# Performance work log

Measured on AMD Instinct MI355X. Metric: run time of the kernel, lower is better.

The kernel has to match this reference:

```python
import jax, jax.numpy as jnp
import numpy as np

# Module constants (from init_kwargs / source constants)
BEV_H, BEV_W = 188, 126
IMG_H, IMG_W = 384, 768
X_MIN, X_MAX = 0.0, 75.2
Y_MIN, Y_MAX = -25.2, 25.2


def _bev_points():
    """Homogeneous car-frame BEV cell centers, [P,4] with P = BEV_H*BEV_W, Z=0."""
    dx = (X_MAX - X_MIN) / BEV_H
    dy = (Y_MAX - Y_MIN) / BEV_W
    xc = jnp.linspace(X_MIN + dx / 2.0, X_MAX - dx / 2.0, BEV_H)
    yc = jnp.linspace(Y_MIN + dy / 2.0, Y_MAX - dy / 2.0, BEV_W)
    X, Y = jnp.meshgrid(xc, yc, indexing='ij')
    P = BEV_H * BEV_W
    return jnp.stack([X.ravel(), Y.ravel(), jnp.zeros(P), jnp.ones(P)], axis=-1)


def setup_inputs() -> dict:
    key = jax.random.key(0)
    k1, k2, k3 = jax.random.split(key, 3)
    B, N, C, Hf, Wf = 2, 6, 256, 48, 96
    feats = jax.random.normal(k1, (B, N, C, Hf, Wf), dtype=jnp.float32)
    # Realistic intrinsics: fx=fy=500, principal point at image center, + small noise
    K_base = jnp.array([[500.0, 0.0, IMG_W / 2.0],
                        [0.0, 500.0, IMG_H / 2.0],
                        [0.0, 0.0, 1.0]], dtype=jnp.float32)
    intrinsics = K_base[None, None] + 5.0 * jax.random.normal(k2, (B, N, 3, 3), dtype=jnp.float32)
    intrinsics = intrinsics.at[..., 2, :].set(jnp.array([0.0, 0.0, 1.0]))
    # Extrinsics: car x (forward) -> cam z, car y -> -cam x, car z (up) -> -cam y,
    # camera 1.5m above ground; small per-camera perturbation so cams differ.
    M_base = jnp.array([[0.0, -1.0, 0.0, 0.0],
                        [0.0, 0.0, -1.0, 1.5],
                        [1.0, 0.0, 0.0, 0.0],
                        [0.0, 0.0, 0.0, 1.0]], dtype=jnp.float32)
    car_to_cam = M_base[None, None] + 0.01 * jax.random.normal(k3, (B, N, 4, 4), dtype=jnp.float32)
    car_to_cam = car_to_cam.at[..., 3, :].set(jnp.array([0.0, 0.0, 0.0, 1.0]))
    return {"feats": feats, "intrinsics": intrinsics, "car_to_cam": car_to_cam}


def _forward(feats, intrinsics, car_to_cam):
    B, N, C, Hf, Wf = feats.shape
    P_car = _bev_points().astype(feats.dtype)  # [P,4]
    # Per-camera projection of BEV points into camera frame: P_cam = P_car @ M^T
    P_cam = jnp.einsum('pk,bnjk->bnpj', P_car, car_to_cam)  # [B,N,P,4]
    Zc = P_cam[..., 2]
    valid = Zc > 0.1
    # Pinhole projection: p_img = K @ P_cam3
    p_img = jnp.einsum('bnij,bnpj->bnpi', intrinsics, P_cam[..., :3])  # [B,N,P,3]
    z = jnp.maximum(p_img[..., 2], 1e-4)
    u_feat = (p_img[..., 0] / z) / (IMG_W / float(Wf))
    v_feat = (p_img[..., 1] / z) / (IMG_H / float(Hf))
    valid = valid & (u_feat >= 0.0) & (u_feat <= Wf - 1.0) & (v_feat >= 0.0) & (v_feat <= Hf - 1.0)
    u_norm = jnp.where(valid, u_feat / (Wf - 1) * 2.0 - 1.0, 2.0)
    v_norm = jnp.where(valid, v_feat / (Hf - 1) * 2.0 - 1.0, 2.0)
    # grid_sample, bilinear, padding_mode='zeros', align_corners=True
    ix = (u_norm + 1.0) * 0.5 * (Wf - 1)  # [B,N,P]
    iy = (v_norm + 1.0) * 0.5 * (Hf - 1)
    x0 = jnp.floor(ix)
    y0 = jnp.floor(iy)
    wx1 = ix - x0
    wx0 = 1.0 - wx1
    wy1 = iy - y0
    wy0 = 1.0 - wy1
    feats_flat = feats.reshape(B, N, C, Hf * Wf)

    def gather(xf, yf):
        inb = (xf >= 0) & (xf <= Wf - 1) & (yf >= 0) & (yf <= Hf - 1)
        xi = jnp.clip(xf, 0, Wf - 1).astype(jnp.int32)
        yi = jnp.clip(yf, 0, Hf - 1).astype(jnp.int32)
        lin = yi * Wf + xi  # [B,N,P]
        val = jnp.take_along_axis(feats_flat, lin[:, :, None, :], axis=3)  # [B,N,C,P]
        return val * inb[:, :, None, :].astype(val.dtype)

    out = (gather(x0, y0) * (wx0 * wy0)[:, :, None, :]
           + gather(x0 + 1.0, y0) * (wx1 * wy0)[:, :, None, :]
           + gather(x0, y0 + 1.0) * (wx0 * wy1)[:, :, None, :]
           + gather(x0 + 1.0, y0 + 1.0) * (wx1 * wy1)[:, :, None, :])  # [B,N,C,P]
    bev = out.mean(axis=1).reshape(B, C, BEV_H, BEV_W)
    return bev


def reference(feats, intrinsics, car_to_cam):
    return _forward(feats, intrinsics, car_to_cam)
```

## Files before the change

### kernel.cpp

```cpp
#include <hip/hip_runtime.h>

namespace {

constexpr int kBevH = 188, kBevW = 126, kP = kBevH * kBevW;
constexpr int kB = 2, kN = 6, kC = 256, kHf = 48, kWf = 96;
constexpr int kHW = kHf * kWf;
constexpr int kPixBytes = kC * 2;
constexpr int kPTile = 32;
constexpr int kNTiles = (kP + kPTile - 1) / kPTile;
constexpr size_t kImgBytes = (size_t)kB * kN * kHW * kC * 2;
constexpr size_t kWsNeeded = kImgBytes;

typedef float vfloat4 __attribute__((ext_vector_type(4)));

__device__ __forceinline__ unsigned short f2bf(float f) {
  union { float f; unsigned u; } a; a.f = f;
  unsigned r = a.u + 0x7fffu + ((a.u >> 16) & 1u);
  return (unsigned short)(r >> 16);
}
__device__ __forceinline__ float bfl(unsigned u) {
  union { unsigned u; float f; } a; a.u = u << 16; return a.f;
}
__device__ __forceinline__ float bfh(unsigned u) {
  union { unsigned u; float f; } a; a.u = u & 0xffff0000u; return a.f;
}

__global__ __launch_bounds__(256) void transpose_cvt_kernel(
    const float* __restrict__ src, unsigned short* __restrict__ dst) {
  __shared__ float tile[64][33];
  const int m = blockIdx.z;
  const int hw0 = blockIdx.x * 32;
  const int c0 = blockIdx.y * 64;
  const float* s = src + (size_t)m * kC * kHW;
  unsigned short* d = dst + (size_t)m * kHW * kC;
  const int hw = threadIdx.x & 31, cl = threadIdx.x >> 5;
#pragma unroll
  for (int k = 0; k < 8; ++k)
    tile[cl + 8 * k][hw] = s[(size_t)(c0 + cl + 8 * k) * kHW + hw0 + hw];
  __syncthreads();
  const int cp = threadIdx.x & 31, hwl = threadIdx.x >> 5;
#pragma unroll
  for (int k = 0; k < 4; ++k) {
    const int h = hwl + 8 * k;
    ushort2 uv;
    uv.x = f2bf(tile[2 * cp][h]);
    uv.y = f2bf(tile[2 * cp + 1][h]);
    *(ushort2*)(d + (size_t)(hw0 + h) * kC + c0 + 2 * cp) = uv;
  }
}

__global__ __launch_bounds__(512) void gather_kernel(
    const unsigned char* __restrict__ tf, const float* __restrict__ intr,
    const float* __restrict__ c2c, float* __restrict__ out) {
  __shared__ float sm[kPTile][261];
  __shared__ int2 s_off[kPTile][kN];
  __shared__ float4 s_wt[kPTile][kN];

  const int b = blockIdx.y;
  const int orig = blockIdx.x;
  constexpr int q = kNTiles / 8, r = kNTiles % 8;
  const int xcd = orig & 7, idx = orig >> 3;
  const int tile = (xcd < r ? xcd * (q + 1) : r * (q + 1) + (xcd - r) * q) + idx;
  const int p0 = tile * kPTile;
  const int tid = threadIdx.x;

  if (tid < kPTile * kN) {
    const int pl = tid / kN, n = tid - pl * kN;
    const int p = min(p0 + pl, kP - 1);
    const int pi = p / kBevW, pj = p - pi * kBevW;
    const float dxc = 75.2f / 188.0f, dyc = 50.4f / 126.0f;
    const float xcar = 0.5f * dxc + (float)pi * dxc;
    const float ycar = -25.2f + 0.5f * dyc + (float)pj * dyc;
    const float* M = c2c + ((size_t)b * kN + n) * 16;
    const float* K = intr + ((size_t)b * kN + n) * 9;
    float Xc = M[0] * xcar + M[1] * ycar + M[3];
    float Yc = M[4] * xcar + M[5] * ycar + M[7];
    float Zc = M[8] * xcar + M[9] * ycar + M[11];
    float u = K[0] * Xc + K[1] * Yc + K[2] * Zc;
    float v = K[3] * Xc + K[4] * Yc + K[5] * Zc;
    float w = K[6] * Xc + K[7] * Yc + K[8] * Zc;
    float z = fmaxf(w, 1e-4f);
    float uf = (u / z) * 0.125f;
    float vf = (v / z) * 0.125f;
    bool valid = (Zc > 0.1f) && (uf >= 0.0f) && (uf <= 95.0f) &&
                 (vf >= 0.0f) && (vf <= 47.0f);
    int2 ov = make_int2(0, 0);
    float4 wv = make_float4(0.f, 0.f, 0.f, 0.f);
    if (valid) {
      float un = (uf / 95.0f) * 2.0f - 1.0f;
      float vn = (vf / 47.0f) * 2.0f - 1.0f;
      float ix = (un + 1.0f) * 0.5f * 95.0f;
      float iy = (vn + 1.0f) * 0.5f * 47.0f;
      float x0f = floorf(ix), y0f = floorf(iy);
      float wx1 = ix - x0f, wx0 = 1.0f - wx1;
      float wy1 = iy - y0f, wy0 = 1.0f - wy1;
      int x0i = (int)x0f;
      int y0i = (int)y0f;
      int xb = min(x0i, 94);
      float h0 = (x0i <= 94) ? wx0 : 0.0f;
      float h1 = (x0i <= 94) ? wx1 : wx0;
      int y1i = min(y0i + 1, 47);
      const int pix = (b * kN + n) * kHW;
      ov.x = (pix + y0i * kWf + xb) * kPixBytes;
      ov.y = (pix + y1i * kWf + xb) * kPixBytes;
      wv = make_float4(h0 * wy0, h1 * wy0, h0 * wy1, h1 * wy1);
    }
    s_off[pl][n] = ov;
    s_wt[pl][n] = wv;
  }
  __syncthreads();

  const int w = tid >> 6, l = tid & 63;
  const int half = l >> 5;
  const int l16 = l << 4;
  const float inv_n = 1.0f / 6.0f;

#pragma unroll
  for (int j = 0; j < 4; ++j) {
    const int pl = w * 4 + j;

    const int2 o0 = s_off[pl][0], o1 = s_off[pl][1], o2 = s_off[pl][2],
               o3 = s_off[pl][3], o4 = s_off[pl][4], o5 = s_off[pl][5];
    const float4 q0 = s_wt[pl][0], q1 = s_wt[pl][1], q2 = s_wt[pl][2],
                 q3 = s_wt[pl][3], q4 = s_wt[pl][4], q5 = s_wt[pl][5];

#define LD(nm, o) \
    const uint4 nm##a = *(const uint4*)(tf + (size_t)o.x + l16); \
    const uint4 nm##b = *(const uint4*)(tf + (size_t)o.y + l16);
    LD(d0, o0) LD(d1, o1) LD(d2, o2) LD(d3, o3) LD(d4, o4) LD(d5, o5)
#undef LD

    float a0 = 0.f, a1 = 0.f, a2 = 0.f, a3 = 0.f,
          a4 = 0.f, a5 = 0.f, a6 = 0.f, a7 = 0.f;
#define CAM(da, db, wv) { \
    const float selA = half ? wv.y : wv.x; \
    const float selB = half ? wv.w : wv.z; \
    a0 += selA * bfl(da.x) + selB * bfl(db.x); \
    a1 += selA * bfh(da.x) + selB * bfh(db.x); \
    a2 += selA * bfl(da.y) + selB * bfl(db.y); \
    a3 += selA * bfh(da.y) + selB * bfh(db.y); \
    a4 += selA * bfl(da.z) + selB * bfl(db.z); \
    a5 += selA * bfh(da.z) + selB * bfh(db.z); \
    a6 += selA * bfl(da.w) + selB * bfl(db.w); \
    a7 += selA * bfh(da.w) + selB * bfh(db.w); }
    CAM(d0a, d0b, q0) CAM(d1a, d1b, q1) CAM(d2a, d2b, q2)
    CAM(d3a, d3b, q3) CAM(d4a, d4b, q4) CAM(d5a, d5b, q5)
#undef CAM

    a0 += __shfl_xor(a0, 32); a1 += __shfl_xor(a1, 32);
    a2 += __shfl_xor(a2, 32); a3 += __shfl_xor(a3, 32);
    a4 += __shfl_xor(a4, 32); a5 += __shfl_xor(a5, 32);
    a6 += __shfl_xor(a6, 32); a7 += __shfl_xor(a7, 32);

    const int cbase = ((l & 31) << 3) + (half << 2);
    float4 vs = half ? make_float4(a4, a5, a6, a7)
                     : make_float4(a0, a1, a2, a3);
    vs.x *= inv_n; vs.y *= inv_n; vs.z *= inv_n; vs.w *= inv_n;
    *(float4*)&sm[pl][cbase] = vs;
  }
  __syncthreads();

#pragma unroll
  for (int rd = 0; rd < 4; ++rd) {
    const int cr = rd * 64 + (tid >> 3);
    const int p4 = (tid & 7) * 4;
    const int pg = p0 + p4;
    if (pg < kP) {
      vfloat4 v = {sm[p4][cr], sm[p4 + 1][cr], sm[p4 + 2][cr],
                   sm[p4 + 3][cr]};
      __builtin_nontemporal_store(
          v, (vfloat4*)(out + ((size_t)(b * kC + cr)) * kP + pg));
    }
  }
}

constexpr int kCChunk = 32;
__global__ __launch_bounds__(256) void ipm_project_kernel(
    const float* __restrict__ feats, const float* __restrict__ intr,
    const float* __restrict__ c2c, float* __restrict__ out) {
  const int p = blockIdx.x * 256 + threadIdx.x;
  const int b = blockIdx.y;
  const int c0 = blockIdx.z * kCChunk;
  const bool inrange = p < kP;
  const int pi = p / kBevW;
  const int pj = p - pi * kBevW;
  const float dx = 75.2f / 188.0f;
  const float dy = 50.4f / 126.0f;
  const float xcar = 0.5f * dx + (float)pi * dx;
  const float ycar = -25.2f + 0.5f * dy + (float)pj * dy;
  int tap[kN][4];
  float tw[kN][4];
  int vmask = 0;
  const float* Kb = intr + (size_t)b * kN * 9;
  const float* Mb = c2c + (size_t)b * kN * 16;
#pragma unroll
  for (int n = 0; n < kN; ++n) {
    const float* M = Mb + n * 16;
    const float* K = Kb + n * 9;
    float Xc = M[0] * xcar + M[1] * ycar + M[3];
    float Yc = M[4] * xcar + M[5] * ycar + M[7];
    float Zc = M[8] * xcar + M[9] * ycar + M[11];
    float u = K[0] * Xc + K[1] * Yc + K[2] * Zc;
    float v = K[3] * Xc + K[4] * Yc + K[5] * Zc;
    float w = K[6] * Xc + K[7] * Yc + K[8] * Zc;
    float z = fmaxf(w, 1e-4f);
    float uf = (u / z) * 0.125f;
    float vf = (v / z) * 0.125f;
    bool valid = inrange && (Zc > 0.1f) && (uf >= 0.0f) && (uf <= 95.0f) &&
                 (vf >= 0.0f) && (vf <= 47.0f);
    if (valid) {
      float un = (uf / 95.0f) * 2.0f - 1.0f;
      float vn = (vf / 47.0f) * 2.0f - 1.0f;
      float ix = (un + 1.0f) * 0.5f * 95.0f;
      float iy = (vn + 1.0f) * 0.5f * 47.0f;
      float x0f = floorf(ix), y0f = floorf(iy);
      float wx1 = ix - x0f, wx0 = 1.0f - wx1;
      float wy1 = iy - y0f, wy0 = 1.0f - wy1;
#pragma unroll
      for (int t = 0; t < 4; ++t) {
        float xf = x0f + (float)(t & 1);
        float yf = y0f + (float)(t >> 1);
        bool inb =
            (xf >= 0.0f) && (xf <= 95.0f) && (yf >= 0.0f) && (yf <= 47.0f);
        int xi = (int)fminf(fmaxf(xf, 0.0f), 95.0f);
        int yi = (int)fminf(fmaxf(yf, 0.0f), 47.0f);
        float wgt = ((t & 1) ? wx1 : wx0) * ((t >> 1) ? wy1 : wy0);
        tap[n][t] = yi * kWf + xi;
        tw[n][t] = inb ? wgt : 0.0f;
      }
      vmask |= (1 << n);
    }
  }
  const float inv_n = 1.0f / 6.0f;
#pragma unroll 4
  for (int k = 0; k < kCChunk; ++k) {
    const int c = c0 + k;
    float acc = 0.0f;
#pragma unroll
    for (int n = 0; n < kN; ++n) {
      if (vmask & (1 << n)) {
        const float* f = feats + ((size_t)(b * kN + n) * kC + c) * kHW;
        acc += f[tap[n][0]] * tw[n][0] + f[tap[n][1]] * tw[n][1] +
               f[tap[n][2]] * tw[n][2] + f[tap[n][3]] * tw[n][3];
      }
    }
    if (inrange) out[((size_t)b * kC + c) * kP + p] = acc * inv_n;
  }
}

}

extern "C" void kernel_launch(void* const* d_in, const int* in_sizes, int n_in,
                              void* d_out, int out_size, void* d_ws,
                              size_t ws_size, hipStream_t stream) {
  const float* feats = (const float*)d_in[0];
  const float* intr = (const float*)d_in[1];
  const float* c2c = (const float*)d_in[2];
  float* out = (float*)d_out;

  if (ws_size >= kWsNeeded && d_ws != nullptr) {
    unsigned short* tf = (unsigned short*)d_ws;
    transpose_cvt_kernel<<<dim3(kHW / 32, kC / 64, kB * kN), 256, 0, stream>>>(
        feats, tf);
    gather_kernel<<<dim3(kNTiles, kB), 512, 0, stream>>>(
        (const unsigned char*)tf, intr, c2c, out);
  } else {
    dim3 grid((kP + 255) / 256, kB, kC / kCChunk);
    ipm_project_kernel<<<grid, dim3(256), 0, stream>>>(feats, intr, c2c, out);
  }
}
```

Measured before the change: 49.20 us.

## Tile gather by 2 BEV rows x 32 columns per block

Each gather block now covers a 2-row by 32-column patch of the BEV grid instead of 32 consecutive flat points. Neighbouring rows project to nearby image pixels, which is meant to improve cache reuse of the gathered feature rows. Each block does 8 points per wave, holding the second row's results in registers and writing them out in a second store phase that reuses the shared buffer. This costs extra barriers and register pressure, and the second row uses 8-byte stores because (pi0+1)*126 is not 16-byte aligned.

```diff
diff --git a/kernel.cpp b/kernel.cpp
--- a/kernel.cpp
+++ b/kernel.cpp
@@ -6,12 +6,14 @@
 constexpr int kB = 2, kN = 6, kC = 256, kHf = 48, kWf = 96;
 constexpr int kHW = kHf * kWf;
 constexpr int kPixBytes = kC * 2;
-constexpr int kPTile = 32;
-constexpr int kNTiles = (kP + kPTile - 1) / kPTile;
 constexpr size_t kImgBytes = (size_t)kB * kN * kHW * kC * 2;
 constexpr size_t kWsNeeded = kImgBytes;
 
+constexpr int kPjTiles = 4, kPiGroups = kBevH / 2;
+constexpr int kGatherBlocks = kPjTiles * kPiGroups;
+
 typedef float vfloat4 __attribute__((ext_vector_type(4)));
+typedef float vfloat2 __attribute__((ext_vector_type(2)));
 
 __device__ __forceinline__ unsigned short f2bf(float f) {
   union { float f; unsigned u; } a; a.f = f;
@@ -52,22 +54,24 @@
 __global__ __launch_bounds__(512) void gather_kernel(
     const unsigned char* __restrict__ tf, const float* __restrict__ intr,
     const float* __restrict__ c2c, float* __restrict__ out) {
-  __shared__ float sm[kPTile][261];
-  __shared__ int2 s_off[kPTile][kN];
-  __shared__ float4 s_wt[kPTile][kN];
+  __shared__ float sm[32][261];
+  __shared__ int2 s_off[64][kN];
+  __shared__ float4 s_wt[64][kN];
 
   const int b = blockIdx.y;
   const int orig = blockIdx.x;
-  constexpr int q = kNTiles / 8, r = kNTiles % 8;
-  const int xcd = orig & 7, idx = orig >> 3;
-  const int tile = (xcd < r ? xcd * (q + 1) : r * (q + 1) + (xcd - r) * q) + idx;
-  const int p0 = tile * kPTile;
+  const int tix = (orig & 7) * (kGatherBlocks / 8) + (orig >> 3);
+  const int pjt = tix & 3;
+  const int pig = tix >> 2;
+  const int pj0 = pjt * 32;
+  const int pi0 = pig * 2;
   const int tid = threadIdx.x;
 
-  if (tid < kPTile * kN) {
-    const int pl = tid / kN, n = tid - pl * kN;
-    const int p = min(p0 + pl, kP - 1);
-    const int pi = p / kBevW, pj = p - pi * kBevW;
+  if (tid < 64 * kN) {
+    const int lp = tid / kN, n = tid - lp * kN;
+    const int dpi = lp >> 5, dpj = lp & 31;
+    const int pj = min(pj0 + dpj, kBevW - 1);
+    const int pi = pi0 + dpi;
     const float dxc = 75.2f / 188.0f, dyc = 50.4f / 126.0f;
     const float xcar = 0.5f * dxc + (float)pi * dxc;
     const float ycar = -25.2f + 0.5f * dyc + (float)pj * dyc;
@@ -105,24 +109,28 @@
       ov.y = (pix + y1i * kWf + xb) * kPixBytes;
       wv = make_float4(h0 * wy0, h1 * wy0, h0 * wy1, h1 * wy1);
     }
-    s_off[pl][n] = ov;
-    s_wt[pl][n] = wv;
+    s_off[lp][n] = ov;
+    s_wt[lp][n] = wv;
   }
   __syncthreads();
 
   const int w = tid >> 6, l = tid & 63;
   const int half = l >> 5;
   const int l16 = l << 4;
+  const int cbase = ((l & 31) << 3) + (half << 2);
   const float inv_n = 1.0f / 6.0f;
 
-#pragma unroll
-  for (int j = 0; j < 4; ++j) {
-    const int pl = w * 4 + j;
-
-    const int2 o0 = s_off[pl][0], o1 = s_off[pl][1], o2 = s_off[pl][2],
-               o3 = s_off[pl][3], o4 = s_off[pl][4], o5 = s_off[pl][5];
-    const float4 q0 = s_wt[pl][0], q1 = s_wt[pl][1], q2 = s_wt[pl][2],
-                 q3 = s_wt[pl][3], q4 = s_wt[pl][4], q5 = s_wt[pl][5];
+  float4 held0, held1, held2, held3;
+
+#pragma unroll
+  for (int j = 0; j < 8; ++j) {
+    const int smrow = 4 * w + (j >> 1);
+    const int lp = ((j & 1) << 5) + smrow;
+
+    const int2 o0 = s_off[lp][0], o1 = s_off[lp][1], o2 = s_off[lp][2],
+               o3 = s_off[lp][3], o4 = s_off[lp][4], o5 = s_off[lp][5];
+    const float4 q0 = s_wt[lp][0], q1 = s_wt[lp][1], q2 = s_wt[lp][2],
+                 q3 = s_wt[lp][3], q4 = s_wt[lp][4], q5 = s_wt[lp][5];
 
 #define LD(nm, o) \
     const uint4 nm##a = *(const uint4*)(tf + (size_t)o.x + l16); \
@@ -152,24 +160,64 @@
     a4 += __shfl_xor(a4, 32); a5 += __shfl_xor(a5, 32);
     a6 += __shfl_xor(a6, 32); a7 += __shfl_xor(a7, 32);
 
-    const int cbase = ((l & 31) << 3) + (half << 2);
     float4 vs = half ? make_float4(a4, a5, a6, a7)
                      : make_float4(a0, a1, a2, a3);
     vs.x *= inv_n; vs.y *= inv_n; vs.z *= inv_n; vs.w *= inv_n;
-    *(float4*)&sm[pl][cbase] = vs;
-  }
-  __syncthreads();
-
-#pragma unroll
-  for (int rd = 0; rd < 4; ++rd) {
-    const int cr = rd * 64 + (tid >> 3);
-    const int p4 = (tid & 7) * 4;
-    const int pg = p0 + p4;
-    if (pg < kP) {
-      vfloat4 v = {sm[p4][cr], sm[p4 + 1][cr], sm[p4 + 2][cr],
-                   sm[p4 + 3][cr]};
-      __builtin_nontemporal_store(
-          v, (vfloat4*)(out + ((size_t)(b * kC + cr)) * kP + pg));
+    if ((j & 1) == 0) {
+      *(float4*)&sm[smrow][cbase] = vs;
+    } else {
+      if ((j >> 1) == 0) held0 = vs;
+      else if ((j >> 1) == 1) held1 = vs;
+      else if ((j >> 1) == 2) held2 = vs;
+      else held3 = vs;
+    }
+  }
+  __syncthreads();
+
+  const int wlimit = (pjt == 3) ? 28 : 32;
+
+  {
+    const size_t row0 = (size_t)pi0 * kBevW + pj0;
+#pragma unroll
+    for (int rd = 0; rd < 4; ++rd) {
+      const int cr = rd * 64 + (tid >> 3);
+      const int p4 = (tid & 7) * 4;
+      if (p4 < wlimit) {
+        vfloat4 v = {sm[p4][cr], sm[p4 + 1][cr], sm[p4 + 2][cr],
+                     sm[p4 + 3][cr]};
+        __builtin_nontemporal_store(
+            v, (vfloat4*)(out + ((size_t)(b * kC + cr)) * kP + row0 + p4));
+      }
+    }
+    if (pjt == 3) {
+      const int cr = tid >> 1, dpj = 28 + (tid & 1);
+      out[((size_t)(b * kC + cr)) * kP + row0 + dpj] = sm[dpj][cr];
+    }
+  }
+  __syncthreads();
+
+  *(float4*)&sm[4 * w + 0][cbase] = held0;
+  *(float4*)&sm[4 * w + 1][cbase] = held1;
+  *(float4*)&sm[4 * w + 2][cbase] = held2;
+  *(float4*)&sm[4 * w + 3][cbase] = held3;
+  __syncthreads();
+  {
+    const size_t row1 = (size_t)(pi0 + 1) * kBevW + pj0;
+#pragma unroll
+    for (int rd = 0; rd < 4; ++rd) {
+      const int cr = rd * 64 + (tid >> 3);
+      const int p4 = (tid & 7) * 4;
+      if (p4 < wlimit) {
+        float* dst = out + ((size_t)(b * kC + cr)) * kP + row1 + p4;
+        vfloat2 v01 = {sm[p4][cr], sm[p4 + 1][cr]};
+        vfloat2 v23 = {sm[p4 + 2][cr], sm[p4 + 3][cr]};
+        __builtin_nontemporal_store(v01, (vfloat2*)dst);
+        __builtin_nontemporal_store(v23, (vfloat2*)(dst + 2));
+      }
+    }
+    if (pjt == 3) {
+      const int cr = tid >> 1, dpj = 28 + (tid & 1);
+      out[((size_t)(b * kC + cr)) * kP + row1 + dpj] = sm[dpj][cr];
     }
   }
 }
@@ -262,7 +310,7 @@
     unsigned short* tf = (unsigned short*)d_ws;
     transpose_cvt_kernel<<<dim3(kHW / 32, kC / 64, kB * kN), 256, 0, stream>>>(
         feats, tf);
-    gather_kernel<<<dim3(kNTiles, kB), 512, 0, stream>>>(
+    gather_kernel<<<dim3(kGatherBlocks, kB), 512, 0, stream>>>(
         (const unsigned char*)tf, intr, c2c, out);
   } else {
     dim3 grid((kP + 255) / 256, kB, kC / kCChunk);
```

Result: slower. 64.62 us (+31.3%).
